# Optimization experiments

Hardware: AMD Instinct MI355X
Metric: run time of the kernel (lower is better)

The kernel has to match this reference:

```python
import jax, jax.numpy as jnp
import numpy as np

EMBED_DIM = 512
NUM_HEADS = 8
HEAD_DIM = EMBED_DIM // NUM_HEADS
SCALE = 1.0 / HEAD_DIM ** 0.5


def setup_inputs() -> dict:
    key = jax.random.key(0)
    ks = jax.random.split(key, 7)
    B, C, H, W = 8, EMBED_DIM, 32, 32
    x = jax.random.normal(ks[0], (B, C, H, W), dtype=jnp.float32)
    s = 1.0 / np.sqrt(EMBED_DIM)
    return {
        "x": x,
        "ln_gamma": jnp.ones((EMBED_DIM,), jnp.float32),
        "ln_beta": jnp.zeros((EMBED_DIM,), jnp.float32),
        "w_qkv": jax.random.uniform(ks[1], (EMBED_DIM, 3 * EMBED_DIM), jnp.float32, -s, s),
        "b_qkv": jax.random.uniform(ks[2], (3 * EMBED_DIM,), jnp.float32, -s, s),
        "w_proj": jax.random.uniform(ks[3], (EMBED_DIM, EMBED_DIM), jnp.float32, -s, s),
        "b_proj": jax.random.uniform(ks[4], (EMBED_DIM,), jnp.float32, -s, s),
    }


def reference(x, ln_gamma, ln_beta, w_qkv, b_qkv, w_proj, b_proj):
    B, C, H, W = x.shape
    N = H * W
    # LayerNorm over channel dim (applied in NHWC layout in the original)
    xs = x.reshape(B, C, N).transpose(0, 2, 1)  # [B, N, C]
    mu = jnp.mean(xs, axis=-1, keepdims=True)
    var = jnp.mean(jnp.square(xs - mu), axis=-1, keepdims=True)
    xn = (xs - mu) / jnp.sqrt(var + 1e-5) * ln_gamma + ln_beta
    # QKV projection
    qkv = xn @ w_qkv + b_qkv                        # [B, N, 3C]
    qkv = qkv.reshape(B, N, 3, NUM_HEADS, HEAD_DIM)
    q = qkv[:, :, 0].transpose(0, 2, 1, 3)         # [B, h, N, d]
    k = qkv[:, :, 1].transpose(0, 2, 1, 3)
    v = qkv[:, :, 2].transpose(0, 2, 1, 3)
    # Scaled dot-product attention (full N x N scores, as in source)
    attn = jnp.einsum('bhnd,bhmd->bhnm', q, k) * SCALE
    attn = jax.nn.softmax(attn, axis=-1)
    o = jnp.einsum('bhnm,bhmd->bhnd', attn, v)     # [B, h, N, d]
    o = o.transpose(0, 2, 1, 3).reshape(B, N, C)
    # Output projection (dropout is identity in eval)
    o = o @ w_proj + b_proj
    return o.transpose(0, 2, 1).reshape(B, C, H, W)
```

## Files before the change

### kernel.cpp

```cpp
#include <hip/hip_runtime.h>
#include <hip/hip_bf16.h>
#include <math.h>

#define B_   8
#define C_   512
#define NH_  8
#define HD_  64
#define NSP  1024
#define M_   (B_*NSP)
#define NQKV 1536
#define SCALE_ 0.125f
#define S2L_  0.18033688f

typedef __attribute__((ext_vector_type(8))) __bf16 bf16x8;
typedef __attribute__((ext_vector_type(4))) float  f32x4;
typedef __attribute__((ext_vector_type(16))) float f32x16;

__device__ __forceinline__ unsigned short f2bf(float f) {
  unsigned int u = __float_as_uint(f);
  u = u + 0x7fffu + ((u >> 16) & 1u);
  return (unsigned short)(u >> 16);
}

__device__ __forceinline__ unsigned int pk2bf(float a, float b) {
  __hip_bfloat162 t = __float22bfloat162_rn(make_float2(a, b));
  unsigned int u; __builtin_memcpy(&u, &t, 4);
  return u;
}

__device__ __forceinline__ void async16(const unsigned short* g, unsigned short* l) {
  __builtin_amdgcn_global_load_lds(
      (const __attribute__((address_space(1))) void*)g,
      (__attribute__((address_space(3))) void*)l, 16, 0, 0);
}

__global__ void ln_stats_kernel(const float* __restrict__ x,
                                float* __restrict__ psum,
                                float* __restrict__ psum2) {
  int tx = threadIdx.x & 31, ty = threadIdx.x >> 5;
  int cg  = blockIdx.x & 3;
  int nch = (blockIdx.x >> 2) & 31;
  int b   = blockIdx.x >> 7;
  int n0 = nch * 32;
  const float* xp = x + (size_t)b * C_ * NSP + n0 + tx;
  float s = 0.f, s2 = 0.f;
  for (int c = cg * 128 + ty; c < cg * 128 + 128; c += 8) {
    float v = xp[(size_t)c * NSP];
    s += v; s2 += v * v;
  }
  __shared__ float sh_s[8][32], sh_s2[8][32];
  sh_s[ty][tx] = s; sh_s2[ty][tx] = s2;
  __syncthreads();
  if (ty == 0) {
    float S = 0.f, S2 = 0.f;
    for (int j = 0; j < 8; j++) { S += sh_s[j][tx]; S2 += sh_s2[j][tx]; }
    psum [cg * M_ + b * NSP + n0 + tx] = S;
    psum2[cg * M_ + b * NSP + n0 + tx] = S2;
  }
}

__global__ __launch_bounds__(256) void applyw_kernel(
    const float* __restrict__ x, const float* __restrict__ psum,
    const float* __restrict__ psum2, const float* __restrict__ gamma,
    const float* __restrict__ beta, const float* __restrict__ wqkv,
    const float* __restrict__ wproj, unsigned short* __restrict__ xn,
    unsigned short* __restrict__ wqkvT, unsigned short* __restrict__ wprojT) {
  int tid = threadIdx.x;
  __shared__ float tile[64][65];
  int tx = tid & 63, ty = tid >> 6;
  if (blockIdx.x >= 1024) {
    const float* W; unsigned short* WT; int NW, t;
    if (blockIdx.x < 1216) { W = wqkv;  WT = wqkvT;  NW = NQKV; t = blockIdx.x - 1024; }
    else                   { W = wproj; WT = wprojT; NW = C_;   t = blockIdx.x - 1216; }
    int ntiles = NW >> 6;
    int kt = t / ntiles, nt = t - kt * ntiles;
    for (int i = ty; i < 64; i += 4)
      tile[i][tx] = W[(size_t)(kt * 64 + i) * NW + nt * 64 + tx];
    __syncthreads();
    for (int i = ty; i < 64; i += 4)
      WT[(size_t)(nt * 64 + i) * C_ + kt * 64 + tx] = f2bf(tile[tx][i]);
    return;
  }
  __shared__ float smu[64], srs[64];
  int c0 = (blockIdx.x & 7) * 64;
  int n0 = ((blockIdx.x >> 3) & 15) * 64;
  int b  = blockIdx.x >> 7;
  if (tid < 64) {
    int n = b * NSP + n0 + tid;
    float s  = psum [n] + psum [M_ + n] + psum [2 * M_ + n] + psum [3 * M_ + n];
    float s2 = psum2[n] + psum2[M_ + n] + psum2[2 * M_ + n] + psum2[3 * M_ + n];
    float mu = s * (1.0f / C_);
    float var = s2 * (1.0f / C_) - mu * mu;
    smu[tid] = mu;
    srs[tid] = rsqrtf(var + 1e-5f);
  }
  const float* xp = x + ((size_t)b * C_ + c0) * NSP + n0;
  for (int i = ty; i < 64; i += 4)
    tile[i][tx] = xp[(size_t)i * NSP + tx];
  __syncthreads();
  float g = gamma[c0 + tx], be = beta[c0 + tx];
  unsigned short* op = xn + ((size_t)(b * NSP + n0)) * C_ + c0 + tx;
  for (int i = ty; i < 64; i += 4) {
    float v = (tile[tx][i] - smu[i]) * srs[i] * g + be;
    op[(size_t)i * C_] = f2bf(v);
  }
}

__global__ __launch_bounds__(256, 3) void gemm_qkv_kernel(
    const unsigned short* __restrict__ A,
    const unsigned short* __restrict__ Bt,
    const float* __restrict__ bias,
    unsigned short* __restrict__ out0, unsigned short* __restrict__ out1) {
  __shared__ __align__(16) char smem[32768];
  int tid = threadIdx.x;
  int wave = tid >> 6, lane = tid & 63, quad = lane >> 4, l15 = lane & 15;
  int n0 = blockIdx.x * 128, m0 = blockIdx.y * 128;
  int wm = (wave >> 1) * 64, wn = (wave & 1) * 64;
  int srow = lane >> 2, schunk = (lane & 3) * 8;
  auto stage = [&](int k0, int buf) {
    unsigned short* As = (unsigned short*)(smem + buf * 16384);
    unsigned short* Bs = (unsigned short*)(smem + buf * 16384 + 8192);
#pragma unroll
    for (int j = 0; j < 2; j++) {
      int r0 = (wave + 4 * j) * 16;
      async16(A + (size_t)(m0 + r0 + srow) * 512 + k0 + schunk, As + r0 * 32 + lane * 8);
      async16(Bt + (size_t)(n0 + r0 + srow) * 512 + k0 + schunk, Bs + r0 * 32 + lane * 8);
    }
  };
  f32x4 acc[4][4] = {};
  stage(0, 0);
  for (int kt = 0; kt < 16; kt++) {
    int cur = kt & 1;
    __syncthreads();
    if (kt < 15) stage((kt + 1) * 32, cur ^ 1);
    unsigned short* As = (unsigned short*)(smem + cur * 16384);
    unsigned short* Bs = (unsigned short*)(smem + cur * 16384 + 8192);
    bf16x8 a[4], bb[4];
#pragma unroll
    for (int mt = 0; mt < 4; mt++)
      a[mt] = *(const bf16x8*)(As + (wm + mt * 16 + l15) * 32 + quad * 8);
#pragma unroll
    for (int nt = 0; nt < 4; nt++)
      bb[nt] = *(const bf16x8*)(Bs + (wn + nt * 16 + l15) * 32 + quad * 8);
#pragma unroll
    for (int mt = 0; mt < 4; mt++)
#pragma unroll
      for (int nt = 0; nt < 4; nt++)
        acc[mt][nt] = __builtin_amdgcn_mfma_f32_16x16x32_bf16(
            a[mt], bb[nt], acc[mt][nt], 0, 0, 0);
  }
  __syncthreads();
  float bw[4];
#pragma unroll
  for (int nt = 0; nt < 4; nt++) bw[nt] = bias[n0 + wn + nt * 16 + l15];
  if (n0 < 1024) {
    float sc = ((n0 + wn) < 512) ? S2L_ : 1.0f;
    unsigned short* buf = (unsigned short*)(smem + wave * 8192);
#pragma unroll
    for (int p = 0; p < 2; p++) {
#pragma unroll
      for (int mh = 0; mh < 2; mh++) {
        int mt = p * 2 + mh;
#pragma unroll
        for (int nt = 0; nt < 4; nt++)
#pragma unroll
          for (int r = 0; r < 4; r++)
            buf[(mh * 16 + quad * 4 + r) * 68 + nt * 16 + l15] =
                f2bf((acc[mt][nt][r] + bw[nt]) * sc);
      }
#pragma unroll
      for (int i = 0; i < 4; i++) {
        int row = i * 8 + (lane >> 3);
        const unsigned short* bp_ = &buf[row * 68 + (lane & 7) * 8];
        uint2 lo = *(const uint2*)bp_;
        uint2 hi = *(const uint2*)(bp_ + 4);
        *(uint4*)(out0 + (size_t)(m0 + wm + p * 32 + row) * 1024 +
                  n0 + wn + (lane & 7) * 8) = make_uint4(lo.x, lo.y, hi.x, hi.y);
      }
    }
  } else {
    unsigned short* buf = (unsigned short*)(smem + wave * 8192);
    int b = m0 >> 10, nbase = m0 & 1023;
    for (int nc = 0; nc < 4; nc++) {
#pragma unroll
      for (int mt = 0; mt < 4; mt++)
#pragma unroll
        for (int r = 0; r < 4; r++)
          buf[(mt * 16 + quad * 4 + r) * 17 + l15] = f2bf(acc[mt][nc][r] + bw[nc]);
#pragma unroll
      for (int cl = 0; cl < 16; cl++) {
        int crel = n0 - 1024 + wn + nc * 16 + cl;
        out1[((size_t)b * C_ + crel) * NSP + nbase + wm + lane] = buf[lane * 17 + cl];
      }
    }
  }
}

__global__ __launch_bounds__(256) void gemm_proj_kernel(
    const unsigned short* __restrict__ A,
    const unsigned short* __restrict__ Bt,
    const float* __restrict__ bias,
    float* __restrict__ O) {
  __shared__ __align__(16) char smem[24576];
  int tid = threadIdx.x;
  int wave = tid >> 6, lane = tid & 63, quad = lane >> 4, l15 = lane & 15;
  int n0 = blockIdx.x * 128, m0 = blockIdx.y * 64;
  int wm = (wave >> 1) * 32, wn = (wave & 1) * 64;
  int srow = lane >> 2, schunk = (lane & 3) * 8;
  auto stage = [&](int k0, int buf) {
    unsigned short* As = (unsigned short*)(smem + buf * 12288);
    unsigned short* Bs = (unsigned short*)(smem + buf * 12288 + 4096);
    async16(A + (size_t)(m0 + wave * 16 + srow) * 512 + k0 + schunk,
            As + wave * 16 * 32 + lane * 8);
#pragma unroll
    for (int j = 0; j < 2; j++) {
      int r0 = (wave + 4 * j) * 16;
      async16(Bt + (size_t)(n0 + r0 + srow) * 512 + k0 + schunk, Bs + r0 * 32 + lane * 8);
    }
  };
  f32x4 acc[2][4] = {};
  stage(0, 0);
  for (int kt = 0; kt < 16; kt++) {
    int cur = kt & 1;
    __syncthreads();
    if (kt < 15) stage((kt + 1) * 32, cur ^ 1);
    unsigned short* As = (unsigned short*)(smem + cur * 12288);
    unsigned short* Bs = (unsigned short*)(smem + cur * 12288 + 4096);
    bf16x8 a[2], bb[4];
#pragma unroll
    for (int mt = 0; mt < 2; mt++)
      a[mt] = *(const bf16x8*)(As + (wm + mt * 16 + l15) * 32 + quad * 8);
#pragma unroll
    for (int nt = 0; nt < 4; nt++)
      bb[nt] = *(const bf16x8*)(Bs + (wn + nt * 16 + l15) * 32 + quad * 8);
#pragma unroll
    for (int mt = 0; mt < 2; mt++)
#pragma unroll
      for (int nt = 0; nt < 4; nt++)
        acc[mt][nt] = __builtin_amdgcn_mfma_f32_16x16x32_bf16(
            a[mt], bb[nt], acc[mt][nt], 0, 0, 0);
  }
  __syncthreads();
  float bw[4];
#pragma unroll
  for (int nt = 0; nt < 4; nt++) bw[nt] = bias[n0 + wn + nt * 16 + l15];
  float* buf = (float*)(smem + wave * 6144);
  int b = m0 >> 10, nbase = m0 & 1023;
  int ml = lane & 31, cg = lane >> 5;
  for (int nc = 0; nc < 4; nc++) {
#pragma unroll
    for (int mt = 0; mt < 2; mt++)
#pragma unroll
      for (int r = 0; r < 4; r++)
        buf[(mt * 16 + quad * 4 + r) * 17 + l15] = acc[mt][nc][r] + bw[nc];
#pragma unroll
    for (int j = 0; j < 8; j++) {
      int cl = j * 2 + cg;
      int c = n0 + wn + nc * 16 + cl;
      O[((size_t)b * C_ + c) * NSP + nbase + wm + ml] = buf[ml * 17 + cl];
    }
  }
}

__global__ __launch_bounds__(256, 1) void attn_kernel(
    const unsigned short* __restrict__ qk,
    const unsigned short* __restrict__ vt,
    unsigned short* __restrict__ o_ws) {
  __shared__ __align__(16) unsigned short Ks[2][64][64];
  __shared__ __align__(16) unsigned short Vts[2][64][64];
  int tid = threadIdx.x;
  int wave = tid >> 6, lane = tid & 63;
  int l31 = lane & 31, hi = lane >> 5;
  int b = blockIdx.x >> 3, h = blockIdx.x & 7;
  int qb = blockIdx.y * 256 + wave * 64;
  int sc8 = lane & 7, sr8 = lane >> 3;
  int swz = sc8 ^ sr8;
  bf16x8 bq[2][4];
#pragma unroll
  for (int qs = 0; qs < 2; qs++)
#pragma unroll
    for (int ks = 0; ks < 4; ks++)
      bq[qs][ks] = *(const bf16x8*)(
          qk + (size_t)(b * NSP + qb + qs * 32 + l31) * 1024 +
          h * 64 + ks * 16 + hi * 8);
  auto stage = [&](int it, int buf) {
    int k0 = it * 64;
#pragma unroll
    for (int g = 0; g < 2; g++) {
      int row = wave * 16 + g * 8 + sr8;
      async16(qk + (size_t)(b * NSP + k0 + row) * 1024 + 512 + h * 64 + swz * 8,
              &Ks[buf][wave * 16 + g * 8][0]);
      async16(vt + ((size_t)(b * C_ + h * 64 + row)) * NSP + k0 + swz * 8,
              &Vts[buf][wave * 16 + g * 8][0]);
    }
  };
  f32x16 ot[2][2] = {};
  float lsum[2] = {0.f, 0.f};
  stage(0, 0);
  for (int it = 0; it < 16; it++) {
    int cur = it & 1;
    __syncthreads();
    if (it < 15) stage(it + 1, cur ^ 1);
    bf16x8 bp[2][4];
#pragma unroll
    for (int kt = 0; kt < 2; kt++) {
      bf16x8 ak[4];
#pragma unroll
      for (int ks = 0; ks < 4; ks++)
        ak[ks] = *(const bf16x8*)(
            &Ks[cur][kt * 32 + l31][((ks * 2 + hi) ^ (l31 & 7)) * 8]);
#pragma unroll
      for (int qs = 0; qs < 2; qs++) {
        f32x16 s = {};
#pragma unroll
        for (int ks = 0; ks < 4; ks++)
          s = __builtin_amdgcn_mfma_f32_32x32x16_bf16(ak[ks], bq[qs][ks], s, 0, 0, 0);
        float p0 = __builtin_amdgcn_exp2f(s[0]),  p1 = __builtin_amdgcn_exp2f(s[1]);
        float p2 = __builtin_amdgcn_exp2f(s[2]),  p3 = __builtin_amdgcn_exp2f(s[3]);
        float p4 = __builtin_amdgcn_exp2f(s[4]),  p5 = __builtin_amdgcn_exp2f(s[5]);
        float p6 = __builtin_amdgcn_exp2f(s[6]),  p7 = __builtin_amdgcn_exp2f(s[7]);
        float p8 = __builtin_amdgcn_exp2f(s[8]),  p9 = __builtin_amdgcn_exp2f(s[9]);
        float pa = __builtin_amdgcn_exp2f(s[10]), pb = __builtin_amdgcn_exp2f(s[11]);
        float pc = __builtin_amdgcn_exp2f(s[12]), pd = __builtin_amdgcn_exp2f(s[13]);
        float pe = __builtin_amdgcn_exp2f(s[14]), pf = __builtin_amdgcn_exp2f(s[15]);
        lsum[qs] += ((p0 + p1) + (p2 + p3)) + ((p4 + p5) + (p6 + p7)) +
                    (((p8 + p9) + (pa + pb)) + ((pc + pd) + (pe + pf)));
        unsigned int d0 = pk2bf(p0, p1), d1 = pk2bf(p2, p3);
        unsigned int d2 = pk2bf(p4, p5), d3 = pk2bf(p6, p7);
        unsigned int d4 = pk2bf(p8, p9), d5 = pk2bf(pa, pb);
        unsigned int d6 = pk2bf(pc, pd), d7 = pk2bf(pe, pf);
        asm volatile("v_permlane32_swap_b32 %0, %1" : "+v"(d0), "+v"(d2));
        asm volatile("v_permlane32_swap_b32 %0, %1" : "+v"(d1), "+v"(d3));
        asm volatile("v_permlane32_swap_b32 %0, %1" : "+v"(d4), "+v"(d6));
        asm volatile("v_permlane32_swap_b32 %0, %1" : "+v"(d5), "+v"(d7));
        uint4 f0 = make_uint4(d0, d1, d2, d3);
        uint4 f1 = make_uint4(d4, d5, d6, d7);
        __builtin_memcpy(&bp[qs][kt * 2 + 0], &f0, 16);
        __builtin_memcpy(&bp[qs][kt * 2 + 1], &f1, 16);
      }
    }
#pragma unroll
    for (int kc = 0; kc < 4; kc++) {
      bf16x8 av0 = *(const bf16x8*)(
          &Vts[cur][l31][((kc * 2 + hi) ^ (l31 & 7)) * 8]);
      bf16x8 av1 = *(const bf16x8*)(
          &Vts[cur][32 + l31][((kc * 2 + hi) ^ (l31 & 7)) * 8]);
#pragma unroll
      for (int qs = 0; qs < 2; qs++) {
        ot[qs][0] = __builtin_amdgcn_mfma_f32_32x32x16_bf16(av0, bp[qs][kc], ot[qs][0], 0, 0, 0);
        ot[qs][1] = __builtin_amdgcn_mfma_f32_32x32x16_bf16(av1, bp[qs][kc], ot[qs][1], 0, 0, 0);
      }
    }
  }
#pragma unroll
  for (int qs = 0; qs < 2; qs++) {
    float lv = __shfl(lsum[qs], l31) + __shfl(lsum[qs], l31 + 32);
    float inv = 1.f / lv;
    unsigned short* orow = o_ws + (size_t)(b * NSP + qb + qs * 32 + l31) * 512 + h * 64;
#pragma unroll
    for (int g = 0; g < 4; g++) {
      int d0 = 8 * g + 4 * hi;
      *(uint2*)(orow + d0) =
          make_uint2(pk2bf(ot[qs][0][4 * g + 0] * inv, ot[qs][0][4 * g + 1] * inv),
                     pk2bf(ot[qs][0][4 * g + 2] * inv, ot[qs][0][4 * g + 3] * inv));
      *(uint2*)(orow + 32 + d0) =
          make_uint2(pk2bf(ot[qs][1][4 * g + 0] * inv, ot[qs][1][4 * g + 1] * inv),
                     pk2bf(ot[qs][1][4 * g + 2] * inv, ot[qs][1][4 * g + 3] * inv));
    }
  }
}

extern "C" void kernel_launch(void* const* d_in, const int* in_sizes, int n_in,
                              void* d_out, int out_size, void* d_ws, size_t ws_size,
                              hipStream_t stream) {
  const float* x     = (const float*)d_in[0];
  const float* gamma = (const float*)d_in[1];
  const float* beta  = (const float*)d_in[2];
  const float* wqkv  = (const float*)d_in[3];
  const float* bqkv  = (const float*)d_in[4];
  const float* wproj = (const float*)d_in[5];
  const float* bproj = (const float*)d_in[6];
  char* ws = (char*)d_ws;
  float*          psum   = (float*)ws;
  float*          psum2  = (float*)(ws + 131072);
  unsigned short* wqkvT  = (unsigned short*)(ws + 262144);
  unsigned short* wprojT = (unsigned short*)(ws + 1835008);
  unsigned short* qk_bf  = (unsigned short*)(ws + 2359296);
  unsigned short* vt_bf  = (unsigned short*)(ws + 19136512);
  unsigned short* xn_bf  = (unsigned short*)(ws + 27525120);
  unsigned short* o_bf   = xn_bf;
  float* out = (float*)d_out;

  ln_stats_kernel<<<1024, 256, 0, stream>>>(x, psum, psum2);
  applyw_kernel<<<1024 + 192 + 64, 256, 0, stream>>>(x, psum, psum2, gamma, beta,
                                                     wqkv, wproj, xn_bf, wqkvT, wprojT);
  gemm_qkv_kernel<<<dim3(NQKV / 128, M_ / 128), 256, 0, stream>>>(
      xn_bf, wqkvT, bqkv, qk_bf, vt_bf);
  attn_kernel<<<dim3(B_ * NH_, NSP / 256), 256, 0, stream>>>(qk_bf, vt_bf, o_bf);
  gemm_proj_kernel<<<dim3(C_ / 128, M_ / 64), 256, 0, stream>>>(
      o_bf, wprojT, bproj, out);
}
```

Measured before the change: 159.5 us.

## Split attention keys across wave pairs and merge partial outputs via LDS

The attention kernel now gives each block 128 queries instead of 256, with two wave pairs each handling half of the 1024 keys (split-K). Partial outputs and row sums are combined through shared memory at the end, and launch bounds allow two blocks per CU. This doubles the grid from 256 to 512 blocks so more CUs are busy and the serial loop per wave is halved, at the cost of a reduction step, more LDS and tighter register limits. The softmax skips max subtraction, so adding partial sums directly is valid.

```diff
diff --git a/kernel.cpp b/kernel.cpp
--- a/kernel.cpp
+++ b/kernel.cpp
@@ -262,17 +262,18 @@
   }
 }
 
-__global__ __launch_bounds__(256, 1) void attn_kernel(
+__global__ __launch_bounds__(256, 2) void attn_kernel(
     const unsigned short* __restrict__ qk,
     const unsigned short* __restrict__ vt,
     unsigned short* __restrict__ o_ws) {
-  __shared__ __align__(16) unsigned short Ks[2][64][64];
-  __shared__ __align__(16) unsigned short Vts[2][64][64];
+  __shared__ __align__(16) unsigned short Ks[2][2][64][64];
+  __shared__ __align__(16) unsigned short Vts[2][2][64][64];
   int tid = threadIdx.x;
   int wave = tid >> 6, lane = tid & 63;
   int l31 = lane & 31, hi = lane >> 5;
+  int qw = wave & 1, kh = wave >> 1;
   int b = blockIdx.x >> 3, h = blockIdx.x & 7;
-  int qb = blockIdx.y * 256 + wave * 64;
+  int qb = blockIdx.y * 128 + qw * 64;
   int sc8 = lane & 7, sr8 = lane >> 3;
   int swz = sc8 ^ sr8;
   bf16x8 bq[2][4];
@@ -284,23 +285,23 @@
           qk + (size_t)(b * NSP + qb + qs * 32 + l31) * 1024 +
           h * 64 + ks * 16 + hi * 8);
   auto stage = [&](int it, int buf) {
-    int k0 = it * 64;
-#pragma unroll
-    for (int g = 0; g < 2; g++) {
-      int row = wave * 16 + g * 8 + sr8;
-      async16(qk + (size_t)(b * NSP + k0 + row) * 1024 + 512 + h * 64 + swz * 8,
-              &Ks[buf][wave * 16 + g * 8][0]);
-      async16(vt + ((size_t)(b * C_ + h * 64 + row)) * NSP + k0 + swz * 8,
-              &Vts[buf][wave * 16 + g * 8][0]);
+    int k0 = kh * 512 + it * 64;
+#pragma unroll
+    for (int g = 0; g < 4; g++) {
+      int row = qw * 32 + g * 8;
+      async16(qk + (size_t)(b * NSP + k0 + row + sr8) * 1024 + 512 + h * 64 + swz * 8,
+              &Ks[buf][kh][row][0]);
+      async16(vt + ((size_t)(b * C_ + h * 64 + row + sr8)) * NSP + k0 + swz * 8,
+              &Vts[buf][kh][row][0]);
     }
   };
   f32x16 ot[2][2] = {};
   float lsum[2] = {0.f, 0.f};
   stage(0, 0);
-  for (int it = 0; it < 16; it++) {
+  for (int it = 0; it < 8; it++) {
     int cur = it & 1;
     __syncthreads();
-    if (it < 15) stage(it + 1, cur ^ 1);
+    if (it < 7) stage(it + 1, cur ^ 1);
     bf16x8 bp[2][4];
 #pragma unroll
     for (int kt = 0; kt < 2; kt++) {
@@ -308,7 +309,7 @@
 #pragma unroll
       for (int ks = 0; ks < 4; ks++)
         ak[ks] = *(const bf16x8*)(
-            &Ks[cur][kt * 32 + l31][((ks * 2 + hi) ^ (l31 & 7)) * 8]);
+            &Ks[cur][kh][kt * 32 + l31][((ks * 2 + hi) ^ (l31 & 7)) * 8]);
 #pragma unroll
       for (int qs = 0; qs < 2; qs++) {
         f32x16 s = {};
@@ -342,9 +343,9 @@
 #pragma unroll
     for (int kc = 0; kc < 4; kc++) {
       bf16x8 av0 = *(const bf16x8*)(
-          &Vts[cur][l31][((kc * 2 + hi) ^ (l31 & 7)) * 8]);
+          &Vts[cur][kh][l31][((kc * 2 + hi) ^ (l31 & 7)) * 8]);
       bf16x8 av1 = *(const bf16x8*)(
-          &Vts[cur][32 + l31][((kc * 2 + hi) ^ (l31 & 7)) * 8]);
+          &Vts[cur][kh][32 + l31][((kc * 2 + hi) ^ (l31 & 7)) * 8]);
 #pragma unroll
       for (int qs = 0; qs < 2; qs++) {
         ot[qs][0] = __builtin_amdgcn_mfma_f32_32x32x16_bf16(av0, bp[qs][kc], ot[qs][0], 0, 0, 0);
@@ -352,20 +353,48 @@
       }
     }
   }
-#pragma unroll
-  for (int qs = 0; qs < 2; qs++) {
-    float lv = __shfl(lsum[qs], l31) + __shfl(lsum[qs], l31 + 32);
-    float inv = 1.f / lv;
-    unsigned short* orow = o_ws + (size_t)(b * NSP + qb + qs * 32 + l31) * 512 + h * 64;
-#pragma unroll
-    for (int g = 0; g < 4; g++) {
-      int d0 = 8 * g + 4 * hi;
-      *(uint2*)(orow + d0) =
-          make_uint2(pk2bf(ot[qs][0][4 * g + 0] * inv, ot[qs][0][4 * g + 1] * inv),
-                     pk2bf(ot[qs][0][4 * g + 2] * inv, ot[qs][0][4 * g + 3] * inv));
-      *(uint2*)(orow + 32 + d0) =
-          make_uint2(pk2bf(ot[qs][1][4 * g + 0] * inv, ot[qs][1][4 * g + 1] * inv),
-                     pk2bf(ot[qs][1][4 * g + 2] * inv, ot[qs][1][4 * g + 3] * inv));
+  __syncthreads();
+  float* Cb = (float*)&Ks[0][0][0][0];
+  float* Lb = (float*)&Vts[0][0][0][0];
+  if (kh == 1) {
+#pragma unroll
+    for (int qs = 0; qs < 2; qs++) {
+#pragma unroll
+      for (int dh = 0; dh < 2; dh++) {
+        int base = ((qw * 2 + qs) * 2 + dh) * 1024;
+#pragma unroll
+        for (int e = 0; e < 16; e++)
+          Cb[base + e * 64 + lane] = ot[qs][dh][e];
+      }
+      Lb[(qw * 2 + qs) * 64 + lane] = lsum[qs];
+    }
+  }
+  __syncthreads();
+  if (kh == 0) {
+#pragma unroll
+    for (int qs = 0; qs < 2; qs++) {
+#pragma unroll
+      for (int dh = 0; dh < 2; dh++) {
+        int base = ((qw * 2 + qs) * 2 + dh) * 1024;
+#pragma unroll
+        for (int e = 0; e < 16; e++)
+          ot[qs][dh][e] += Cb[base + e * 64 + lane];
+      }
+      float lo = lsum[qs] + Lb[(qw * 2 + qs) * 64 + lane];
+      float lv = __shfl(lo, l31) + __shfl(lo, l31 + 32);
+      float inv = 1.f / lv;
+      unsigned short* orow =
+          o_ws + (size_t)(b * NSP + qb + qs * 32 + l31) * 512 + h * 64;
+#pragma unroll
+      for (int g = 0; g < 4; g++) {
+        int d0 = 8 * g + 4 * hi;
+        *(uint2*)(orow + d0) =
+            make_uint2(pk2bf(ot[qs][0][4 * g + 0] * inv, ot[qs][0][4 * g + 1] * inv),
+                       pk2bf(ot[qs][0][4 * g + 2] * inv, ot[qs][0][4 * g + 3] * inv));
+        *(uint2*)(orow + 32 + d0) =
+            make_uint2(pk2bf(ot[qs][1][4 * g + 0] * inv, ot[qs][1][4 * g + 1] * inv),
+                       pk2bf(ot[qs][1][4 * g + 2] * inv, ot[qs][1][4 * g + 3] * inv));
+      }
     }
   }
 }
@@ -396,7 +425,7 @@
                                                      wqkv, wproj, xn_bf, wqkvT, wprojT);
   gemm_qkv_kernel<<<dim3(NQKV / 128, M_ / 128), 256, 0, stream>>>(
       xn_bf, wqkvT, bqkv, qk_bf, vt_bf);
-  attn_kernel<<<dim3(B_ * NH_, NSP / 256), 256, 0, stream>>>(qk_bf, vt_bf, o_bf);
+  attn_kernel<<<dim3(B_ * NH_, NSP / 128), 256, 0, stream>>>(qk_bf, vt_bf, o_bf);
   gemm_proj_kernel<<<dim3(C_ / 128, M_ / 64), 256, 0, stream>>>(
       o_bf, wprojT, bproj, out);
 }
```

Result: faster. 149.8 us (-6.1%).
